# Performance work log

Measured on AMD Instinct MI355X. Metric: run time of the kernel, lower is better.

Reference implementation:

```python
import jax, jax.numpy as jnp
import numpy as np

L, D, H, DK, FF, R, N, B = 8, 256, 8, 32, 1024, 37, 1024, 1
EPS = 1e-6


def setup_inputs() -> dict:
    key = jax.random.key(0)
    ks = jax.random.split(key, 16)
    def w(i, shape, s=0.05):
        return jax.random.normal(ks[i], shape, jnp.float32) * s
    return {
        "x": jax.random.normal(ks[0], (B, N, D), jnp.float32),
        "relations": jax.random.randint(ks[1], (N, N), 0, R),
        "Wq": w(2, (L, D, D)), "bq": jnp.zeros((L, D), jnp.float32),
        "Wk": w(3, (L, D, D)), "bk": jnp.zeros((L, D), jnp.float32),
        "Wv": w(4, (L, D, D)), "bv": jnp.zeros((L, D), jnp.float32),
        "Wo": w(5, (L, D, D)), "bo": jnp.zeros((L, D), jnp.float32),
        "rel_k_emb": w(6, (L, R, DK)), "rel_v_emb": w(7, (L, R, DK)),
        "W1": w(8, (L, D, FF)), "b1": jnp.zeros((L, FF), jnp.float32),
        "W2": w(9, (L, FF, D)), "b2": jnp.zeros((L, D), jnp.float32),
        "ln1_g": jnp.ones((L, D), jnp.float32), "ln1_b": jnp.zeros((L, D), jnp.float32),
        "ln2_g": jnp.ones((L, D), jnp.float32), "ln2_b": jnp.zeros((L, D), jnp.float32),
        "lnf_g": jnp.ones((D,), jnp.float32), "lnf_b": jnp.zeros((D,), jnp.float32),
    }


def _layernorm(h, g, b):
    # Annotated-Transformer LayerNorm: g*(x-mu)/(std+eps)+b with unbiased std
    mu = h.mean(-1, keepdims=True)
    sd = jnp.sqrt(h.var(-1, keepdims=True, ddof=1))
    return g * (h - mu) / (sd + EPS) + b


def reference(x, relations, Wq, bq, Wk, bk, Wv, bv, Wo, bo,
              rel_k_emb, rel_v_emb, W1, b1, W2, b2,
              ln1_g, ln1_b, ln2_g, ln2_b, lnf_g, lnf_b):
    Bb, n, d = x.shape
    scale = 1.0 / jnp.sqrt(jnp.float32(DK))
    for l in range(L):
        # --- relation-aware self-attention sublayer (pre-norm residual) ---
        xn = _layernorm(x, ln1_g[l], ln1_b[l])
        q = (xn @ Wq[l] + bq[l]).reshape(Bb, n, H, DK).transpose(0, 2, 1, 3)
        k = (xn @ Wk[l] + bk[l]).reshape(Bb, n, H, DK).transpose(0, 2, 1, 3)
        v = (xn @ Wv[l] + bv[l]).reshape(Bb, n, H, DK).transpose(0, 2, 1, 3)
        rk = rel_k_emb[l][relations]  # [n, n, DK] irregular gather
        rv = rel_v_emb[l][relations]  # [n, n, DK]
        scores = (jnp.einsum('bhid,bhjd->bhij', q, k)
                  + jnp.einsum('bhid,ijd->bhij', q, rk)) * scale
        p = jax.nn.softmax(scores, axis=-1)
        o = (jnp.einsum('bhij,bhjd->bhid', p, v)
             + jnp.einsum('bhij,ijd->bhid', p, rv))
        o = o.transpose(0, 2, 1, 3).reshape(Bb, n, d) @ Wo[l] + bo[l]
        x = x + o
        # --- position-wise FFN sublayer (pre-norm residual) ---
        xn = _layernorm(x, ln2_g[l], ln2_b[l])
        x = x + (jax.nn.relu(xn @ W1[l] + b1[l]) @ W2[l] + b2[l])
    return _layernorm(x, lnf_g, lnf_b)
```

## Files before the change

### kernel.cpp

```cpp
#include <hip/hip_runtime.h>
#include <stdint.h>

#define L_ 8
#define D_ 256
#define H_ 8
#define DK_ 32
#define FF_ 1024
#define R_ 37
#define N_ 1024

#define SCL (0.17677669529663689f * 1.4426950408889634f)

typedef float f4v __attribute__((ext_vector_type(4)));
typedef short b8v __attribute__((ext_vector_type(8)));

__device__ __forceinline__ ushort f2b(float f){
  union { float f; uint32_t u; } x; x.f = f;
  return (ushort)((x.u + 0x7FFFu + ((x.u >> 16) & 1u)) >> 16);
}
__device__ __forceinline__ float b2f(ushort u){
  union { uint32_t u; float f; } x; x.u = ((uint32_t)u) << 16;
  return x.f;
}
__device__ __forceinline__ ushort f2h(float f){
  union { _Float16 h; ushort u; } x; x.h = (_Float16)f;
  return x.u;
}
__device__ __forceinline__ float h2f(ushort u){
  union { ushort u; _Float16 h; } x; x.u = u;
  return (float)x.h;
}
__device__ __forceinline__ float ex2(float x){ return __builtin_amdgcn_exp2f(x); }

__device__ __forceinline__ void lds_fadd(float* p, float v){
  asm volatile("ds_add_f32 %0, %1" :: "v"((uint)(uintptr_t)p), "v"(v) : "memory");
}

__global__ __launch_bounds__(256)
void wcast_kernel(const float* __restrict__ src, ushort* __restrict__ dst, int K, int Nc){
  __shared__ float t[32][33];
  int l = blockIdx.z;
  long base = (long)l * K * Nc;
  int n0 = blockIdx.x * 32, k0 = blockIdx.y * 32;
  int tx = threadIdx.x, ty = threadIdx.y;
  #pragma unroll
  for (int r = 0; r < 32; r += 8)
    t[ty + r][tx] = src[base + (long)(k0 + ty + r) * Nc + n0 + tx];
  __syncthreads();
  #pragma unroll
  for (int r = 0; r < 32; r += 8)
    dst[base + (long)(n0 + ty + r) * K + k0 + tx] = f2b(t[tx][ty + r]);
}

__global__ __launch_bounds__(256)
void rel8_kernel(const int* __restrict__ rel, uint* __restrict__ rel8){
  long idx = (long)blockIdx.x * 256 + threadIdx.x;
  int4 v = ((const int4*)rel)[idx];
  rel8[idx] = (uint)(v.x & 255) | ((uint)(v.y & 255) << 8)
            | ((uint)(v.z & 255) << 16) | ((uint)(v.w & 255) << 24);
}

template<int OUTB>
__global__ __launch_bounds__(64)
void ln_kernel(const float* __restrict__ x, const float* __restrict__ g, const float* __restrict__ b,
               ushort* __restrict__ ob, float* __restrict__ of){
  int row = blockIdx.x, lane = threadIdx.x;
  float4 v = ((const float4*)(x + (long)row * D_))[lane];
  float s = v.x + v.y + v.z + v.w;
  float s2 = v.x*v.x + v.y*v.y + v.z*v.z + v.w*v.w;
  #pragma unroll
  for (int o = 32; o; o >>= 1){ s += __shfl_xor(s, o); s2 += __shfl_xor(s2, o); }
  float mu = s * (1.f / D_);
  float var = (s2 - D_ * mu * mu) * (1.f / (D_ - 1));
  var = fmaxf(var, 0.f);
  float inv = 1.f / (sqrtf(var) + 1e-6f);
  float4 gv = ((const float4*)g)[lane];
  float4 bv = ((const float4*)b)[lane];
  float o0 = gv.x * (v.x - mu) * inv + bv.x;
  float o1 = gv.y * (v.y - mu) * inv + bv.y;
  float o2 = gv.z * (v.z - mu) * inv + bv.z;
  float o3 = gv.w * (v.w - mu) * inv + bv.w;
  if (OUTB){
    ushort4 u; u.x = f2b(o0); u.y = f2b(o1); u.z = f2b(o2); u.w = f2b(o3);
    ((ushort4*)ob)[(long)row * 64 + lane] = u;
  } else {
    float4 o; o.x = o0; o.y = o1; o.z = o2; o.w = o3;
    ((float4*)of)[(long)row * 64 + lane] = o;
  }
}

template<int QKV, int RELU, int RESID, int OUTF, int OUTB, int OUTH = 0>
__global__ __launch_bounds__(256)
void gemm_kernel(const ushort* __restrict__ A,
                 const ushort* __restrict__ W0, const ushort* __restrict__ W1p, const ushort* __restrict__ W2p,
                 const float* __restrict__ B0, const float* __restrict__ B1p, const float* __restrict__ B2p,
                 float* __restrict__ resid, float* __restrict__ outF, ushort* __restrict__ outB,
                 ushort* __restrict__ outB2,
                 int M, int Nc, int K, long aB, long wB, long oB){
  __shared__ ushort Al[64 * 48];
  __shared__ ushort Bl[64 * 48];
  int tid = threadIdx.x;
  int lane = tid & 63, w = tid >> 6;
  int wm = w >> 1, wn = w & 1;
  int bn0 = blockIdx.x * 64, bm0 = blockIdx.y * 64;
  long zb = blockIdx.z;
  A += zb * aB;
  const ushort* WT; const float* bias; int wn0;
  if (QKV){
    int which = bn0 >> 8;
    WT = which == 0 ? W0 : (which == 1 ? W1p : W2p);
    bias = which == 0 ? B0 : (which == 1 ? B1p : B2p);
    wn0 = bn0 & 255;
  } else { WT = W0; bias = B0; wn0 = bn0; }
  WT += zb * wB;

  int r4 = tid >> 2, c8 = (tid & 3) * 8;
  const ushort* ag = A + (long)(bm0 + r4) * K + c8;
  const ushort* bg = WT + (long)(wn0 + r4) * K + c8;

  f4v acc[2][2];
  #pragma unroll
  for (int i = 0; i < 2; ++i)
    #pragma unroll
    for (int j = 0; j < 2; ++j)
      acc[i][j] = (f4v){0.f, 0.f, 0.f, 0.f};

  int l16 = lane & 15, lg = lane >> 4;
  int arow0 = (wm * 32 + l16) * 48 + lg * 8;
  int brow0 = (wn * 32 + l16) * 48 + lg * 8;

  for (int k0 = 0; k0 < K; k0 += 32){
    b8v a8 = *(const b8v*)(ag + k0);
    b8v b8 = *(const b8v*)(bg + k0);
    __syncthreads();
    *(b8v*)&Al[r4 * 48 + c8] = a8;
    *(b8v*)&Bl[r4 * 48 + c8] = b8;
    __syncthreads();
    b8v a0 = *(const b8v*)&Al[arow0];
    b8v a1 = *(const b8v*)&Al[arow0 + 16 * 48];
    b8v b0 = *(const b8v*)&Bl[brow0];
    b8v b1 = *(const b8v*)&Bl[brow0 + 16 * 48];
    acc[0][0] = __builtin_amdgcn_mfma_f32_16x16x32_bf16(a0, b0, acc[0][0], 0, 0, 0);
    acc[0][1] = __builtin_amdgcn_mfma_f32_16x16x32_bf16(a0, b1, acc[0][1], 0, 0, 0);
    acc[1][0] = __builtin_amdgcn_mfma_f32_16x16x32_bf16(a1, b0, acc[1][0], 0, 0, 0);
    acc[1][1] = __builtin_amdgcn_mfma_f32_16x16x32_bf16(a1, b1, acc[1][1], 0, 0, 0);
  }
  #pragma unroll
  for (int fi = 0; fi < 2; ++fi)
    #pragma unroll
    for (int fj = 0; fj < 2; ++fj){
      int row0 = bm0 + wm * 32 + fi * 16 + lg * 4;
      int col = bn0 + wn * 32 + fj * 16 + l16;
      if (OUTH){
        ushort4 pk;
        pk.x = f2h(acc[fi][fj][0]); pk.y = f2h(acc[fi][fj][1]);
        pk.z = f2h(acc[fi][fj][2]); pk.w = f2h(acc[fi][fj][3]);
        *(ushort4*)(outB + zb * oB + (long)col * 1024 + row0) = pk;
        continue;
      }
      float vv[4];
      #pragma unroll
      for (int j = 0; j < 4; ++j) vv[j] = acc[fi][fj][j] + bias[QKV ? (col & 255) : col];
      if (QKV){
        int which = col >> 8, hh = (col >> 5) & 7, dk = col & 31;
        if (which == 2){
          ushort4 pk; pk.x = f2b(vv[0]); pk.y = f2b(vv[1]); pk.z = f2b(vv[2]); pk.w = f2b(vv[3]);
          *(ushort4*)(outB2 + (long)hh * 32768 + (long)dk * 1024 + row0) = pk;
        } else {
          #pragma unroll
          for (int j = 0; j < 4; ++j)
            outB[(long)which * 262144 + (long)hh * 32768 + (long)(row0 + j) * 32 + dk] = f2b(vv[j]);
        }
      } else {
        #pragma unroll
        for (int j = 0; j < 4; ++j){
          float v = vv[j];
          if (RELU) v = fmaxf(v, 0.f);
          long idx = (long)(row0 + j) * Nc + col;
          if (RESID) v += resid[idx];
          if (OUTF) outF[idx] = v;
          if (OUTB) outB[idx] = f2b(v);
        }
      }
    }
}

__global__ __launch_bounds__(320)
void qr_kernel(const ushort* __restrict__ qb, const float* __restrict__ rke, float* __restrict__ qr){
  __shared__ float ql[256];
  int i = blockIdx.x, t = threadIdx.x;
  if (t < 256){
    int h = t >> 5, dk = t & 31;
    ql[t] = b2f(qb[(long)((h << 10) + i) * 32 + dk]);
  }
  __syncthreads();
  if (t < H_ * R_){
    int h = t / R_, r = t - h * R_;
    const float* qh = &ql[h * DK_];
    const float* e = rke + r * DK_;
    float acc = 0.f;
    #pragma unroll
    for (int d = 0; d < DK_; ++d) acc += qh[d] * e[d];
    qr[((long)(h << 10) + i) * 40 + r] = acc * SCL;
  }
}

__global__ __launch_bounds__(256)
void sm_kernel(const ushort* __restrict__ S, const float* __restrict__ qr,
               const unsigned char* __restrict__ rel8, const float* __restrict__ rve,
               ushort* __restrict__ P, float* __restrict__ o2){
  __shared__ float qrl[4][40];
  __shared__ float bins[4][44];
  int tid = threadIdx.x, lane = tid & 63, w = tid >> 6;
  int h = blockIdx.y, i = blockIdx.x * 4 + w;
  long rowq = (long)(h << 10) + i;

  if (lane < 40) qrl[w][lane] = qr[rowq * 40 + lane];
  if (lane < 44) bins[w][lane] = 0.f;

  const ushort* Srow = S + rowq * 1024 + lane * 16;
  b8v s0 = *(const b8v*)Srow;
  b8v s1 = *(const b8v*)(Srow + 8);
  uint4 rr = *(const uint4*)(rel8 + (long)i * 1024 + lane * 16);
  uint rw[4] = { rr.x, rr.y, rr.z, rr.w };

  int rix[16];
  #pragma unroll
  for (int q = 0; q < 4; ++q)
    #pragma unroll
    for (int e = 0; e < 4; ++e)
      rix[q * 4 + e] = (rw[q] >> (8 * e)) & 255;

  float sv[16];
  #pragma unroll
  for (int e = 0; e < 8; ++e){
    sv[e]     = h2f((ushort)s0[e]) * SCL + qrl[w][rix[e]];
    sv[8 + e] = h2f((ushort)s1[e]) * SCL + qrl[w][rix[8 + e]];
  }
  float m = sv[0];
  #pragma unroll
  for (int e = 1; e < 16; ++e) m = fmaxf(m, sv[e]);
  #pragma unroll
  for (int o = 1; o < 64; o <<= 1) m = fmaxf(m, __shfl_xor(m, o));

  float p[16], ls = 0.f;
  #pragma unroll
  for (int e = 0; e < 16; ++e){ p[e] = ex2(sv[e] - m); ls += p[e]; }
  #pragma unroll
  for (int o = 1; o < 64; o <<= 1) ls += __shfl_xor(ls, o);
  float rinv = 1.f / ls;

  #pragma unroll
  for (int e = 0; e < 16; ++e) lds_fadd(&bins[w][rix[e]], p[e]);

  b8v po0, po1;
  #pragma unroll
  for (int e = 0; e < 8; ++e){
    po0[e] = (short)f2b(p[e] * rinv);
    po1[e] = (short)f2b(p[8 + e] * rinv);
  }
  *(b8v*)(P + rowq * 1024 + lane * 16) = po0;
  *(b8v*)(P + rowq * 1024 + lane * 16 + 8) = po1;

  int d = lane & 31, half = lane >> 5;
  float acc = 0.f;
  int r0 = half * 19, r1 = r0 + 19 < R_ ? r0 + 19 : R_;
  for (int r = r0; r < r1; ++r) acc += bins[w][r] * rve[r * 32 + d];
  acc += __shfl_xor(acc, 32);
  if (lane < 32) o2[rowq * 32 + d] = acc * rinv;
}

__global__ __launch_bounds__(256)
void pv_kernel(const ushort* __restrict__ P, const ushort* __restrict__ vbt,
               const float* __restrict__ o2, ushort* __restrict__ ob){
  __shared__ ushort Al[64 * 48];
  __shared__ ushort Bl[32 * 48];
  int tid = threadIdx.x, lane = tid & 63, w = tid >> 6;
  int l16 = lane & 15, g = lane >> 4;
  int i0 = blockIdx.x * 64, h = blockIdx.y;
  const ushort* Ph = P + (long)h * 1024 * 1024;
  const ushort* Vh = vbt + (long)h * 32 * 1024;
  int r4 = tid >> 2, c8 = (tid & 3) * 8;

  f4v acc0 = (f4v){0,0,0,0}, acc1 = (f4v){0,0,0,0};
  int arow = (w * 16 + l16) * 48 + g * 8;
  int brow0 = l16 * 48 + g * 8, brow1 = (16 + l16) * 48 + g * 8;

  for (int k0 = 0; k0 < 1024; k0 += 32){
    b8v a8 = *(const b8v*)(Ph + (long)(i0 + r4) * 1024 + k0 + c8);
    b8v b8;
    if (tid < 128) b8 = *(const b8v*)(Vh + (long)r4 * 1024 + k0 + c8);
    __syncthreads();
    *(b8v*)&Al[r4 * 48 + c8] = a8;
    if (tid < 128) *(b8v*)&Bl[r4 * 48 + c8] = b8;
    __syncthreads();
    b8v a0 = *(const b8v*)&Al[arow];
    b8v b0 = *(const b8v*)&Bl[brow0];
    b8v b1 = *(const b8v*)&Bl[brow1];
    acc0 = __builtin_amdgcn_mfma_f32_16x16x32_bf16(a0, b0, acc0, 0, 0, 0);
    acc1 = __builtin_amdgcn_mfma_f32_16x16x32_bf16(a0, b1, acc1, 0, 0, 0);
  }
  #pragma unroll
  for (int e = 0; e < 4; ++e){
    int i = i0 + w * 16 + g * 4 + e;
    long ob2 = ((long)(h << 10) + i) * 32;
    float v0 = acc0[e] + o2[ob2 + l16];
    float v1 = acc1[e] + o2[ob2 + 16 + l16];
    ob[(long)i * 256 + h * 32 + l16] = f2b(v0);
    ob[(long)i * 256 + h * 32 + 16 + l16] = f2b(v1);
  }
}

extern "C" void kernel_launch(void* const* d_in, const int* in_sizes, int n_in,
                              void* d_out, int out_size, void* d_ws, size_t ws_size,
                              hipStream_t stream){
  const float* x    = (const float*)d_in[0];
  const int*   rel  = (const int*)d_in[1];
  const float* Wq   = (const float*)d_in[2];
  const float* bq   = (const float*)d_in[3];
  const float* Wk   = (const float*)d_in[4];
  const float* bk   = (const float*)d_in[5];
  const float* Wv   = (const float*)d_in[6];
  const float* bv   = (const float*)d_in[7];
  const float* Wo   = (const float*)d_in[8];
  const float* bo   = (const float*)d_in[9];
  const float* rke  = (const float*)d_in[10];
  const float* rve  = (const float*)d_in[11];
  const float* W1   = (const float*)d_in[12];
  const float* b1   = (const float*)d_in[13];
  const float* W2   = (const float*)d_in[14];
  const float* b2   = (const float*)d_in[15];
  const float* ln1g = (const float*)d_in[16];
  const float* ln1b = (const float*)d_in[17];
  const float* ln2g = (const float*)d_in[18];
  const float* ln2b = (const float*)d_in[19];
  const float* lnfg = (const float*)d_in[20];
  const float* lnfb = (const float*)d_in[21];

  char* wsb = (char*)d_ws;
  size_t off = 0;
  auto alloc = [&](size_t bytes){ void* p = wsb + off; off += (bytes + 255) & ~255ull; return p; };
  float*  xw   = (float*) alloc((size_t)N_ * D_ * 4);
  ushort* qkvb = (ushort*)alloc((size_t)3 * H_ * N_ * DK_ * 2);
  ushort* vbt  = (ushort*)alloc((size_t)H_ * DK_ * N_ * 2);
  float*  qr   = (float*) alloc((size_t)H_ * N_ * 40 * 4);
  ushort* xnb  = (ushort*)alloc((size_t)N_ * D_ * 2);
  ushort* obf  = (ushort*)alloc((size_t)N_ * D_ * 2);
  ushort* hidb = (ushort*)alloc((size_t)N_ * FF_ * 2);
  uint*   rel8 = (uint*)  alloc((size_t)N_ * N_);
  ushort* Sbuf = (ushort*)alloc((size_t)H_ * N_ * N_ * 2);
  ushort* Pbuf = (ushort*)alloc((size_t)H_ * N_ * N_ * 2);
  float*  o2b  = (float*) alloc((size_t)H_ * N_ * DK_ * 4);
  ushort* wqT  = (ushort*)alloc((size_t)L_ * D_ * D_ * 2);
  ushort* wkT  = (ushort*)alloc((size_t)L_ * D_ * D_ * 2);
  ushort* wvT  = (ushort*)alloc((size_t)L_ * D_ * D_ * 2);
  ushort* woT  = (ushort*)alloc((size_t)L_ * D_ * D_ * 2);
  ushort* w1T  = (ushort*)alloc((size_t)L_ * D_ * FF_ * 2);
  ushort* w2T  = (ushort*)alloc((size_t)L_ * D_ * FF_ * 2);
  (void)ws_size; (void)in_sizes; (void)n_in; (void)out_size;

  ushort* qb = qkvb;
  ushort* kb = qkvb + (size_t)H_ * N_ * DK_;

  dim3 tb(32, 8);
  wcast_kernel<<<dim3(D_/32,  D_/32,  L_), tb, 0, stream>>>(Wq, wqT, D_, D_);
  wcast_kernel<<<dim3(D_/32,  D_/32,  L_), tb, 0, stream>>>(Wk, wkT, D_, D_);
  wcast_kernel<<<dim3(D_/32,  D_/32,  L_), tb, 0, stream>>>(Wv, wvT, D_, D_);
  wcast_kernel<<<dim3(D_/32,  D_/32,  L_), tb, 0, stream>>>(Wo, woT, D_, D_);
  wcast_kernel<<<dim3(FF_/32, D_/32,  L_), tb, 0, stream>>>(W1, w1T, D_, FF_);
  wcast_kernel<<<dim3(D_/32,  FF_/32, L_), tb, 0, stream>>>(W2, w2T, FF_, D_);
  rel8_kernel<<<N_ * N_ / 1024, 256, 0, stream>>>(rel, rel8);

  hipMemcpyAsync(xw, x, (size_t)N_ * D_ * 4, hipMemcpyDeviceToDevice, stream);

  for (int l = 0; l < L_; ++l){
    ln_kernel<1><<<N_, 64, 0, stream>>>(xw, ln1g + l * D_, ln1b + l * D_, xnb, nullptr);
    gemm_kernel<1,0,0,0,1><<<dim3(768/64, N_/64), 256, 0, stream>>>(
        xnb, wqT + (size_t)l * D_ * D_, wkT + (size_t)l * D_ * D_, wvT + (size_t)l * D_ * D_,
        bq + l * D_, bk + l * D_, bv + l * D_,
        nullptr, nullptr, qkvb, vbt, N_, 768, D_, 0, 0, 0);
    qr_kernel<<<N_, 320, 0, stream>>>(qb, rke + (size_t)l * R_ * DK_, qr);
    gemm_kernel<0,0,0,0,0,1><<<dim3(N_/64, N_/64, H_), 256, 0, stream>>>(
        kb, qb, nullptr, nullptr, nullptr, nullptr, nullptr,
        nullptr, nullptr, Sbuf, nullptr, N_, N_, DK_,
        (long)N_ * DK_, (long)N_ * DK_, (long)N_ * N_);
    sm_kernel<<<dim3(N_/4, H_), 256, 0, stream>>>(
        Sbuf, qr, (const unsigned char*)rel8, rve + (size_t)l * R_ * DK_, Pbuf, o2b);
    pv_kernel<<<dim3(N_/64, H_), 256, 0, stream>>>(Pbuf, vbt, o2b, obf);
    gemm_kernel<0,0,1,1,0><<<dim3(D_/64, N_/64), 256, 0, stream>>>(
        obf, woT + (size_t)l * D_ * D_, nullptr, nullptr,
        bo + l * D_, nullptr, nullptr,
        xw, xw, nullptr, nullptr, N_, D_, D_, 0, 0, 0);
    ln_kernel<1><<<N_, 64, 0, stream>>>(xw, ln2g + l * D_, ln2b + l * D_, xnb, nullptr);
    gemm_kernel<0,1,0,0,1><<<dim3(FF_/64, N_/64), 256, 0, stream>>>(
        xnb, w1T + (size_t)l * D_ * FF_, nullptr, nullptr,
        b1 + l * FF_, nullptr, nullptr,
        nullptr, nullptr, hidb, nullptr, N_, FF_, D_, 0, 0, 0);
    gemm_kernel<0,0,1,1,0><<<dim3(D_/64, N_/64), 256, 0, stream>>>(
        hidb, w2T + (size_t)l * FF_ * D_, nullptr, nullptr,
        b2 + l * D_, nullptr, nullptr,
        xw, xw, nullptr, nullptr, N_, D_, FF_, 0, 0, 0);
  }
  ln_kernel<0><<<N_, 64, 0, stream>>>(xw, lnfg, lnfb, nullptr, (float*)d_out);
}
```

Measured before the change: 943.2 us.

## Fuse softmax and PV into one kernel keeping P in LDS

Merges the softmax kernel and the P·V MFMA kernel into a single spv_kernel. Each 512-thread block computes softmax for 32 rows, stores the bf16 probabilities in LDS, and runs the PV product from there with a split-K over four wave pairs reduced through shared memory. The relation-value term is folded into the epilogue. This removes the global round trip of the 16MB P buffer and the o2 buffer, plus one launch per layer. In exchange the block uses a large LDS footprint (about 90KB), which limits occupancy, and adds more syncthreads in the K loop.

```diff
diff --git a/kernel.cpp b/kernel.cpp
--- a/kernel.cpp
+++ b/kernel.cpp
@@ -205,109 +205,128 @@
   }
 }
 
-__global__ __launch_bounds__(256)
-void sm_kernel(const ushort* __restrict__ S, const float* __restrict__ qr,
-               const unsigned char* __restrict__ rel8, const float* __restrict__ rve,
-               ushort* __restrict__ P, float* __restrict__ o2){
-  __shared__ float qrl[4][40];
-  __shared__ float bins[4][44];
-  int tid = threadIdx.x, lane = tid & 63, w = tid >> 6;
-  int h = blockIdx.y, i = blockIdx.x * 4 + w;
-  long rowq = (long)(h << 10) + i;
-
-  if (lane < 40) qrl[w][lane] = qr[rowq * 40 + lane];
-  if (lane < 44) bins[w][lane] = 0.f;
-
-  const ushort* Srow = S + rowq * 1024 + lane * 16;
-  b8v s0 = *(const b8v*)Srow;
-  b8v s1 = *(const b8v*)(Srow + 8);
-  uint4 rr = *(const uint4*)(rel8 + (long)i * 1024 + lane * 16);
-  uint rw[4] = { rr.x, rr.y, rr.z, rr.w };
-
-  int rix[16];
-  #pragma unroll
-  for (int q = 0; q < 4; ++q)
-    #pragma unroll
-    for (int e = 0; e < 4; ++e)
-      rix[q * 4 + e] = (rw[q] >> (8 * e)) & 255;
-
-  float sv[16];
-  #pragma unroll
-  for (int e = 0; e < 8; ++e){
-    sv[e]     = h2f((ushort)s0[e]) * SCL + qrl[w][rix[e]];
-    sv[8 + e] = h2f((ushort)s1[e]) * SCL + qrl[w][rix[8 + e]];
-  }
-  float m = sv[0];
-  #pragma unroll
-  for (int e = 1; e < 16; ++e) m = fmaxf(m, sv[e]);
-  #pragma unroll
-  for (int o = 1; o < 64; o <<= 1) m = fmaxf(m, __shfl_xor(m, o));
-
-  float p[16], ls = 0.f;
-  #pragma unroll
-  for (int e = 0; e < 16; ++e){ p[e] = ex2(sv[e] - m); ls += p[e]; }
-  #pragma unroll
-  for (int o = 1; o < 64; o <<= 1) ls += __shfl_xor(ls, o);
-  float rinv = 1.f / ls;
-
-  #pragma unroll
-  for (int e = 0; e < 16; ++e) lds_fadd(&bins[w][rix[e]], p[e]);
-
-  b8v po0, po1;
-  #pragma unroll
-  for (int e = 0; e < 8; ++e){
-    po0[e] = (short)f2b(p[e] * rinv);
-    po1[e] = (short)f2b(p[8 + e] * rinv);
-  }
-  *(b8v*)(P + rowq * 1024 + lane * 16) = po0;
-  *(b8v*)(P + rowq * 1024 + lane * 16 + 8) = po1;
-
-  int d = lane & 31, half = lane >> 5;
-  float acc = 0.f;
-  int r0 = half * 19, r1 = r0 + 19 < R_ ? r0 + 19 : R_;
-  for (int r = r0; r < r1; ++r) acc += bins[w][r] * rve[r * 32 + d];
-  acc += __shfl_xor(acc, 32);
-  if (lane < 32) o2[rowq * 32 + d] = acc * rinv;
-}
-
-__global__ __launch_bounds__(256)
-void pv_kernel(const ushort* __restrict__ P, const ushort* __restrict__ vbt,
-               const float* __restrict__ o2, ushort* __restrict__ ob){
-  __shared__ ushort Al[64 * 48];
-  __shared__ ushort Bl[32 * 48];
+#define PST 1048
+__global__ __launch_bounds__(512)
+void spv_kernel(const ushort* __restrict__ S, const float* __restrict__ qr,
+                const unsigned char* __restrict__ rel8, const float* __restrict__ rve,
+                const ushort* __restrict__ vbt, ushort* __restrict__ ob){
+  __shared__ ushort P_l[32 * PST];
+  __shared__ ushort Bl[4][32 * 48];
+  __shared__ float part[2][4][16 * 33];
+  __shared__ float qr_l[32 * 40];
+  __shared__ float rvl[R_ * 32];
+  __shared__ float binsw[8][8 * 41];
+  __shared__ float binsout[32 * 41];
+
   int tid = threadIdx.x, lane = tid & 63, w = tid >> 6;
   int l16 = lane & 15, g = lane >> 4;
-  int i0 = blockIdx.x * 64, h = blockIdx.y;
-  const ushort* Ph = P + (long)h * 1024 * 1024;
-  const ushort* Vh = vbt + (long)h * 32 * 1024;
-  int r4 = tid >> 2, c8 = (tid & 3) * 8;
-
+  int i0 = blockIdx.x * 32, h = blockIdx.y;
+
+  for (int idx = tid; idx < 32 * 40; idx += 512)
+    qr_l[idx] = qr[((long)(h << 10) + i0) * 40 + idx];
+  for (int idx = tid; idx < R_ * 32; idx += 512) rvl[idx] = rve[idx];
+  for (int idx = tid; idx < 8 * 8 * 41; idx += 512) ((float*)binsw)[idx] = 0.f;
+  __syncthreads();
+
+  b8v s0[4], s1[4];
+  uint4 rr4[4];
+  #pragma unroll
+  for (int r = 0; r < 4; ++r){
+    long rowq = (long)(h << 10) + i0 + w * 4 + r;
+    const ushort* Sr = S + rowq * 1024 + lane * 16;
+    s0[r] = *(const b8v*)Sr;
+    s1[r] = *(const b8v*)(Sr + 8);
+    rr4[r] = *(const uint4*)(rel8 + (long)(i0 + w * 4 + r) * 1024 + lane * 16);
+  }
+  #pragma unroll
+  for (int r = 0; r < 4; ++r){
+    int row = w * 4 + r;
+    uint rw[4] = { rr4[r].x, rr4[r].y, rr4[r].z, rr4[r].w };
+    int rix[16];
+    #pragma unroll
+    for (int q = 0; q < 4; ++q)
+      #pragma unroll
+      for (int e = 0; e < 4; ++e)
+        rix[q * 4 + e] = (rw[q] >> (8 * e)) & 255;
+    float sv[16];
+    #pragma unroll
+    for (int e = 0; e < 8; ++e){
+      sv[e]     = h2f((ushort)s0[r][e]) * SCL + qr_l[row * 40 + rix[e]];
+      sv[8 + e] = h2f((ushort)s1[r][e]) * SCL + qr_l[row * 40 + rix[8 + e]];
+    }
+    float m = sv[0];
+    #pragma unroll
+    for (int e = 1; e < 16; ++e) m = fmaxf(m, sv[e]);
+    #pragma unroll
+    for (int o = 1; o < 64; o <<= 1) m = fmaxf(m, __shfl_xor(m, o));
+    float p[16], ls = 0.f;
+    #pragma unroll
+    for (int e = 0; e < 16; ++e){ p[e] = ex2(sv[e] - m); ls += p[e]; }
+    #pragma unroll
+    for (int o = 1; o < 64; o <<= 1) ls += __shfl_xor(ls, o);
+    float rinv = 1.f / ls;
+
+    float* bc = &binsw[w][(lane >> 3) * 41];
+    #pragma unroll
+    for (int e = 0; e < 16; ++e) lds_fadd(&bc[rix[e]], p[e]);
+
+    b8v po0, po1;
+    #pragma unroll
+    for (int e = 0; e < 8; ++e){
+      po0[e] = (short)f2b(p[e] * rinv);
+      po1[e] = (short)f2b(p[8 + e] * rinv);
+    }
+    *(b8v*)&P_l[row * PST + lane * 16] = po0;
+    *(b8v*)&P_l[row * PST + lane * 16 + 8] = po1;
+
+    if (lane < R_){
+      float b = 0.f;
+      #pragma unroll
+      for (int c = 0; c < 8; ++c) b += binsw[w][c * 41 + lane];
+      binsout[row * 41 + lane] = b * rinv;
+    }
+    #pragma unroll
+    for (int c = 0; c < 8; ++c)
+      if (lane < 41) binsw[w][c * 41 + lane] = 0.f;
+  }
+  __syncthreads();
+
+  int rg = w & 1, kq = w >> 1;
   f4v acc0 = (f4v){0,0,0,0}, acc1 = (f4v){0,0,0,0};
-  int arow = (w * 16 + l16) * 48 + g * 8;
+  int arowbase = (rg * 16 + l16) * PST + g * 8;
   int brow0 = l16 * 48 + g * 8, brow1 = (16 + l16) * 48 + g * 8;
-
-  for (int k0 = 0; k0 < 1024; k0 += 32){
-    b8v a8 = *(const b8v*)(Ph + (long)(i0 + r4) * 1024 + k0 + c8);
-    b8v b8;
-    if (tid < 128) b8 = *(const b8v*)(Vh + (long)r4 * 1024 + k0 + c8);
+  int sq = tid >> 7, st = tid & 127;
+  int sr4 = st >> 2, sc8 = (st & 3) * 8;
+  const ushort* vsrc = vbt + (long)h * 32768 + (long)sr4 * 1024 + sq * 256 + sc8;
+
+  for (int t = 0; t < 8; ++t){
+    *(b8v*)&Bl[sq][sr4 * 48 + sc8] = *(const b8v*)(vsrc + t * 32);
     __syncthreads();
-    *(b8v*)&Al[r4 * 48 + c8] = a8;
-    if (tid < 128) *(b8v*)&Bl[r4 * 48 + c8] = b8;
-    __syncthreads();
-    b8v a0 = *(const b8v*)&Al[arow];
-    b8v b0 = *(const b8v*)&Bl[brow0];
-    b8v b1 = *(const b8v*)&Bl[brow1];
+    int k0 = kq * 256 + t * 32;
+    b8v a0 = *(const b8v*)&P_l[arowbase + k0];
+    b8v b0 = *(const b8v*)&Bl[kq][brow0];
+    b8v b1 = *(const b8v*)&Bl[kq][brow1];
     acc0 = __builtin_amdgcn_mfma_f32_16x16x32_bf16(a0, b0, acc0, 0, 0, 0);
     acc1 = __builtin_amdgcn_mfma_f32_16x16x32_bf16(a0, b1, acc1, 0, 0, 0);
+    __syncthreads();
   }
   #pragma unroll
   for (int e = 0; e < 4; ++e){
-    int i = i0 + w * 16 + g * 4 + e;
-    long ob2 = ((long)(h << 10) + i) * 32;
-    float v0 = acc0[e] + o2[ob2 + l16];
-    float v1 = acc1[e] + o2[ob2 + 16 + l16];
-    ob[(long)i * 256 + h * 32 + l16] = f2b(v0);
-    ob[(long)i * 256 + h * 32 + 16 + l16] = f2b(v1);
+    part[rg][kq][(g * 4 + e) * 33 + l16] = acc0[e];
+    part[rg][kq][(g * 4 + e) * 33 + 16 + l16] = acc1[e];
+  }
+  __syncthreads();
+
+  for (int slot = tid; slot < 1024; slot += 512){
+    int row = slot >> 5, d = slot & 31;
+    int rg2 = row >> 4, rl = row & 15;
+    float o = 0.f;
+    #pragma unroll
+    for (int q = 0; q < 4; ++q) o += part[rg2][q][rl * 33 + d];
+    float o2 = 0.f;
+    #pragma unroll
+    for (int r = 0; r < R_; ++r) o2 += binsout[row * 41 + r] * rvl[r * 32 + d];
+    ob[(long)(i0 + row) * 256 + h * 32 + d] = f2b(o + o2);
   }
 }
 
@@ -349,8 +368,6 @@
   ushort* hidb = (ushort*)alloc((size_t)N_ * FF_ * 2);
   uint*   rel8 = (uint*)  alloc((size_t)N_ * N_);
   ushort* Sbuf = (ushort*)alloc((size_t)H_ * N_ * N_ * 2);
-  ushort* Pbuf = (ushort*)alloc((size_t)H_ * N_ * N_ * 2);
-  float*  o2b  = (float*) alloc((size_t)H_ * N_ * DK_ * 4);
   ushort* wqT  = (ushort*)alloc((size_t)L_ * D_ * D_ * 2);
   ushort* wkT  = (ushort*)alloc((size_t)L_ * D_ * D_ * 2);
   ushort* wvT  = (ushort*)alloc((size_t)L_ * D_ * D_ * 2);
@@ -384,9 +401,8 @@
         kb, qb, nullptr, nullptr, nullptr, nullptr, nullptr,
         nullptr, nullptr, Sbuf, nullptr, N_, N_, DK_,
         (long)N_ * DK_, (long)N_ * DK_, (long)N_ * N_);
-    sm_kernel<<<dim3(N_/4, H_), 256, 0, stream>>>(
-        Sbuf, qr, (const unsigned char*)rel8, rve + (size_t)l * R_ * DK_, Pbuf, o2b);
-    pv_kernel<<<dim3(N_/64, H_), 256, 0, stream>>>(Pbuf, vbt, o2b, obf);
+    spv_kernel<<<dim3(N_/32, H_), 512, 0, stream>>>(
+        Sbuf, qr, (const unsigned char*)rel8, rve + (size_t)l * R_ * DK_, vbt, obf);
     gemm_kernel<0,0,1,1,0><<<dim3(D_/64, N_/64), 256, 0, stream>>>(
         obf, woT + (size_t)l * D_ * D_, nullptr, nullptr,
         bo + l * D_, nullptr, nullptr,
```

Result: faster. 887.6 us (-5.9%).
